# Performance work log

Measured on AMD Instinct MI355X. Metric: run time of the kernel, lower is better.

The kernel has to match this reference:

```python
import jax, jax.numpy as jnp
import numpy as np

DIM = 512
NUM_HEADS = 8


def setup_inputs() -> dict:
    key = jax.random.key(0)
    ks = jax.random.split(key, 10)
    B, N, C = 2, 4096, DIM
    s = 0.02
    return {
        "x": jax.random.normal(ks[0], (B, N, C), dtype=jnp.float32),
        "Wq": jax.random.normal(ks[1], (C, C), dtype=jnp.float32) * s,
        "Wk": jax.random.normal(ks[2], (C, C), dtype=jnp.float32) * s,
        "Wv": jax.random.normal(ks[3], (C, C), dtype=jnp.float32) * s,
        "Wattn": jax.random.normal(ks[4], (C, C), dtype=jnp.float32) * s,
        "Wconv": jax.random.normal(ks[5], (C, C), dtype=jnp.float32) * s,
        "dw_kernel": jax.random.normal(ks[6], (C, 1, 3), dtype=jnp.float32) * s,  # depthwise (O, I/groups, K)
        "dw_bias": jax.random.normal(ks[7], (C,), dtype=jnp.float32) * s,
        "Wcout": jax.random.normal(ks[8], (C, C), dtype=jnp.float32) * s,
        "H": 8,
        "W": 512,
    }


def reference(x, Wq, Wk, Wv, Wattn, Wconv, dw_kernel, dw_bias, Wcout, H, W):
    B, N, C = x.shape
    nh = NUM_HEADS
    hd = C // nh
    scale = hd ** (-0.5)

    # QKV projections (torch Linear: x @ W.T), split heads -> [B, nh, N, hd]
    q = (x @ Wq.T).reshape(B, N, nh, hd).transpose(0, 2, 1, 3)
    k = (x @ Wk.T).reshape(B, N, nh, hd).transpose(0, 2, 1, 3)
    v = (x @ Wv.T).reshape(B, N, nh, hd).transpose(0, 2, 1, 3)

    # Materialized N x N attention (faithful to source)
    scores = jnp.einsum("bhqd,bhkd->bhqk", q, k) * scale
    weights = jax.nn.softmax(scores, axis=-1)
    attn = jnp.einsum("bhqk,bhkd->bhqd", weights, v)
    attn = attn.transpose(0, 2, 1, 3).reshape(B, N, C)
    attn_out = attn @ Wattn.T

    # Parallel depthwise-conv branch
    ci = (x @ Wconv.T).transpose(0, 2, 1)  # [B, C, N]
    co = jax.lax.conv_general_dilated(
        ci, dw_kernel,
        window_strides=(1,), padding=((1, 1),),
        feature_group_count=C,
        dimension_numbers=("NCH", "OIH", "NCH"),
    ) + dw_bias[None, :, None]
    conv_out = co.transpose(0, 2, 1) @ Wcout.T  # [B, N, C]

    out = attn_out + conv_out
    # NOTE: source shadows arg H with num_heads before the view
    return out.reshape(B, nh, W, C)
```

## Files before the change

### kernel.cpp

```cpp
#include <hip/hip_runtime.h>

typedef __attribute__((ext_vector_type(8))) short bf16x8;
typedef __attribute__((ext_vector_type(4))) float f32x4;

constexpr int kB = 2, kN = 4096, kC = 512, kNH = 8, kHD = 64;
constexpr int kBN = kB * kN;
constexpr int kWElems = 262144;
constexpr int kWAll = 6 * kWElems;
constexpr int kWExtra = 3584;
constexpr float kQScale = 0.1803368801f;

__device__ __forceinline__ short f2bf(float f) {
  union { float f; unsigned u; } v; v.f = f;
  unsigned r = v.u + 0x7fffu + ((v.u >> 16) & 1u);
  return (short)(r >> 16);
}
__device__ __forceinline__ float bf2f(short s) {
  union { unsigned u; float f; } v; v.u = ((unsigned)(unsigned short)s) << 16;
  return v.f;
}
__device__ __forceinline__ float exp2_(float x) {
#if __has_builtin(__builtin_amdgcn_exp2f)
  return __builtin_amdgcn_exp2f(x);
#else
  return exp2f(x);
#endif
}
__device__ __forceinline__ unsigned pk2bf(float a, float b) {
  union { float f; unsigned u; } ua, ub; ua.f = a; ub.f = b;
#if __has_builtin(__builtin_amdgcn_perm)
  return __builtin_amdgcn_perm(ub.u + 0x8000u, ua.u + 0x8000u, 0x07060302u);
#else
  return ((ua.u + 0x8000u) >> 16) | (((ub.u + 0x8000u) >> 16) << 16);
#endif
}

__device__ __forceinline__ bf16x8 ld8(const short* p) { return *(const bf16x8*)p; }
__device__ __forceinline__ bf16x8 ld8(const float* p) {
  float4 a = *(const float4*)p;
  float4 b = *(const float4*)(p + 4);
  bf16x8 r;
  r[0] = f2bf(a.x); r[1] = f2bf(a.y); r[2] = f2bf(a.z); r[3] = f2bf(a.w);
  r[4] = f2bf(b.x); r[5] = f2bf(b.y); r[6] = f2bf(b.z); r[7] = f2bf(b.w);
  return r;
}

__device__ __forceinline__ void gload_lds16(const void* g, void* l) {
  __builtin_amdgcn_global_load_lds(
      (const __attribute__((address_space(1))) void*)g,
      (__attribute__((address_space(3))) void*)l, 16, 0, 0);
}

__global__ void detect_dtype(const unsigned* __restrict__ x, int* __restrict__ flag) {
  const int lane = threadIdx.x & 63;
  unsigned w = x[lane];
  int e = (int)((w >> 7) & 0xffu);
  bool bf = (e >= 100 && e <= 140);
  unsigned long long m = __ballot(bf);
  if (lane == 0) *flag = (__popcll(m) >= 32) ? 1 : 0;
}

constexpr int kW8 = kWAll / 8;
constexpr int kX8 = kBN * kC / 8;
__global__ __launch_bounds__(256) void convert_all(
    const void* Wq, const void* Wk, const void* Wv, const void* Wc,
    const void* Wa, const void* Wco, const void* dwk, const void* dwb,
    const void* x, const int* __restrict__ flag, short* __restrict__ dst,
    short* __restrict__ xb) {
  const int gtid = blockIdx.x * 256 + threadIdx.x;
  const bool bf = (*flag != 0);
  if (gtid < kW8) {
    const int e = gtid * 8;
    const int t = e >> 18, off = e & (kWElems - 1);
    const void* src = (t == 0) ? Wq : (t == 1) ? Wk : (t == 2) ? Wv
                    : (t == 3) ? Wc : (t == 4) ? Wa : Wco;
    bf16x8 v = bf ? ld8((const short*)src + off) : ld8((const float*)src + off);
    *(bf16x8*)(dst + e) = v;
  } else if (gtid < kW8 + kWExtra) {
    const int eoff = gtid - kW8;
    if (eoff < 1536) {
      dst[kWAll + eoff] = bf ? ((const short*)dwk)[eoff]
                             : f2bf(((const float*)dwk)[eoff]);
    } else if (eoff < 2048) {
      const int i = eoff - 1536;
      dst[kWAll + 1536 + i] = bf ? ((const short*)dwb)[i]
                                 : f2bf(((const float*)dwb)[i]);
    } else {
      const int t2 = eoff - 2048;
      const int tap = t2 >> 9, c = t2 & 511;
      dst[kWAll + 2048 + t2] = bf ? ((const short*)dwk)[c * 3 + tap]
                                  : f2bf(((const float*)dwk)[c * 3 + tap]);
    }
  } else if (gtid < kW8 + kWExtra + kX8) {
    const int e = (gtid - kW8 - kWExtra) * 8;
    bf16x8 v = bf ? ld8((const short*)x + e) : ld8((const float*)x + e);
    *(bf16x8*)(xb + e) = v;
  }
}

__global__ __launch_bounds__(256, 3) void proj_gemm(
    const short* __restrict__ xb, const short* __restrict__ wb,
    short* __restrict__ q, short* __restrict__ k, short* __restrict__ vT,
    short* __restrict__ ci) {
  __shared__ __align__(16) short Sh[16384];
  short* As = Sh;
  short* Bs = Sh + 8192;
  const int t = threadIdx.x;
  const int wave = t >> 6, lane = t & 63;
  const int row = lane & 15, quad = lane >> 4;
  const int bn = blockIdx.x & 15;
  const int bm = blockIdx.x >> 4;
  const int m0 = bm * 128, n0 = bn * 128;
  const int wm = wave & 1, wn = wave >> 1;
  const int lrow = lane >> 3, lch = lane & 7;

  f32x4 acc[4][4];
#pragma unroll
  for (int mi = 0; mi < 4; ++mi)
#pragma unroll
    for (int ni = 0; ni < 4; ++ni)
#pragma unroll
      for (int r = 0; r < 4; ++r) acc[mi][ni][r] = 0.0f;

  for (int k0 = 0; k0 < kC; k0 += 64) {
#pragma unroll
    for (int p = 0; p < 4; ++p) {
      const int m = wave * 32 + p * 8 + lrow;
      const int kch = lch ^ (m & 7);
      gload_lds16(xb + (size_t)(m0 + m) * kC + k0 + kch * 8,
                  &As[(wave * 32 + p * 8) * 64]);
      gload_lds16(wb + (size_t)(n0 + m) * kC + k0 + kch * 8,
                  &Bs[(wave * 32 + p * 8) * 64]);
    }
    __syncthreads();

#pragma unroll
    for (int kk2 = 0; kk2 < 2; ++kk2) {
      bf16x8 af[4], bfr[4];
#pragma unroll
      for (int mi = 0; mi < 4; ++mi) {
        const int m = wm * 64 + mi * 16 + row;
        const int ch = (kk2 * 4 + quad) ^ (m & 7);
        af[mi] = *(const bf16x8*)(&As[m * 64 + ch * 8]);
      }
#pragma unroll
      for (int ni = 0; ni < 4; ++ni) {
        const int n = wn * 64 + ni * 16 + row;
        const int ch = (kk2 * 4 + quad) ^ (n & 7);
        bfr[ni] = *(const bf16x8*)(&Bs[n * 64 + ch * 8]);
      }
#pragma unroll
      for (int mi = 0; mi < 4; ++mi)
#pragma unroll
        for (int ni = 0; ni < 4; ++ni)
          acc[mi][ni] = __builtin_amdgcn_mfma_f32_16x16x32_bf16(
              af[mi], bfr[ni], acc[mi][ni], 0, 0, 0);
    }
    __syncthreads();
  }

  const int mat = n0 >> 9;
  const float scale = (mat == 0) ? kQScale : 1.0f;
  if (mat != 2) {
#pragma unroll
    for (int mi = 0; mi < 4; ++mi)
#pragma unroll
      for (int ni = 0; ni < 4; ++ni)
#pragma unroll
        for (int r = 0; r < 4; ++r) {
          const int m = wm * 64 + mi * 16 + quad * 4 + r;
          const int n = wn * 64 + ni * 16 + row;
          Sh[m * 128 + (((n >> 3) ^ (m & 15)) * 8) + (n & 7)] =
              f2bf(acc[mi][ni][r] * scale);
        }
  } else {
#pragma unroll
    for (int mi = 0; mi < 4; ++mi)
#pragma unroll
      for (int ni = 0; ni < 4; ++ni)
#pragma unroll
        for (int r = 0; r < 4; ++r) {
          const int m = wm * 64 + mi * 16 + quad * 4 + r;
          const int n = wn * 64 + ni * 16 + row;
          Sh[n * 128 + (((m >> 3) ^ (n & 15)) * 8) + (m & 7)] =
              f2bf(acc[mi][ni][r]);
        }
  }
  __syncthreads();
  const int b_ = m0 >> 12;
  const int rsub = lane >> 4, chk = lane & 15;
#pragma unroll
  for (int i = 0; i < 8; ++i) {
    const int rr = i * 16 + wave * 4 + rsub;
    bf16x8 v = *(const bf16x8*)(&Sh[rr * 128 + ((chk ^ (rr & 15)) * 8)]);
    if (mat == 2) {
      const int cg = (n0 + rr) & 511;
      const int h = cg >> 6, d = cg & 63;
      const int nb = (m0 & (kN - 1)) + chk * 8;
      *(bf16x8*)(vT + ((size_t)((b_ * kNH + h) * kHD + d)) * kN + nb) = v;
    } else {
      const int n_ = (m0 & (kN - 1)) + rr;
      const int cg = (n0 + chk * 8) & 511;
      if (mat == 3) {
        *(bf16x8*)(ci + ((size_t)(b_ * kN + n_)) * kC + cg) = v;
      } else {
        const int h = cg >> 6, d = cg & 63;
        short* dst = (mat == 0) ? q : k;
        *(bf16x8*)(dst + ((size_t)((b_ * kNH + h) * kN + n_)) * kHD + d) = v;
      }
    }
  }
}

__global__ __launch_bounds__(256) void dwconv(
    const short* __restrict__ ci, const short* __restrict__ wb,
    short* __restrict__ cb) {
  const int e0 = (blockIdx.x * 256 + threadIdx.x) * 8;
  const int c0 = e0 & (kC - 1);
  const int bn = e0 >> 9;
  const int n_ = bn & (kN - 1);
  bf16x8 xc = ld8(ci + e0);
  bf16x8 xm, xp;
  if (n_ > 0) xm = ld8(ci + e0 - kC);
  else
#pragma unroll
    for (int i = 0; i < 8; ++i) xm[i] = 0;
  if (n_ < kN - 1) xp = ld8(ci + e0 + kC);
  else
#pragma unroll
    for (int i = 0; i < 8; ++i) xp[i] = 0;
  bf16x8 w0 = ld8(wb + kWAll + 2048 + c0);
  bf16x8 w1 = ld8(wb + kWAll + 2048 + 512 + c0);
  bf16x8 w2 = ld8(wb + kWAll + 2048 + 1024 + c0);
  bf16x8 bi = ld8(wb + kWAll + 1536 + c0);
  bf16x8 o;
#pragma unroll
  for (int i = 0; i < 8; ++i) {
    float a = bf2f(bi[i]) + bf2f(xm[i]) * bf2f(w0[i]) +
              bf2f(xc[i]) * bf2f(w1[i]) + bf2f(xp[i]) * bf2f(w2[i]);
    o[i] = f2bf(a);
  }
  *(bf16x8*)(cb + e0) = o;
}

__global__ __launch_bounds__(512, 2) void attn_flash(
    const short* __restrict__ q, const short* __restrict__ k,
    const short* __restrict__ vT, short* __restrict__ attn) {
  __shared__ __align__(16) short SMEM[34816];
  short* Kb = SMEM;
  short* Vb = SMEM + 16384;
  const int t = threadIdx.x;
  const int wave = t >> 6;
  const int lane = t & 63;
  const int row = lane & 15;
  const int quad = lane >> 4;
  const int qg = wave & 3;
  const int ks = wave >> 2;

  const int slot = blockIdx.x & 7;
  const int inner = blockIdx.x >> 3;
  const int bh = slot * 2 + (inner & 1);
  const int q0 = (inner >> 1) * 256 + qg * 64;

  const short* qbase = q + (size_t)(bh * kN + q0) * kHD;
  const short* kbase = k + (size_t)bh * kN * kHD;
  const short* vbase = vT + (size_t)bh * kHD * kN;

  bf16x8 qb[4][2];
#pragma unroll
  for (int g = 0; g < 4; ++g) {
    qb[g][0] = *(const bf16x8*)(qbase + (g * 16 + row) * kHD + quad * 8);
    qb[g][1] = *(const bf16x8*)(qbase + (g * 16 + row) * kHD + 32 + quad * 8);
  }

  const f32x4 z4 = {0.0f, 0.0f, 0.0f, 0.0f};

  f32x4 o[4][4];
#pragma unroll
  for (int g = 0; g < 4; ++g)
#pragma unroll
    for (int j = 0; j < 4; ++j)
#pragma unroll
      for (int r = 0; r < 4; ++r) o[g][j][r] = 0.0f;
  float l_[4] = {0.0f, 0.0f, 0.0f, 0.0f};

  const int ksrow = lane >> 3;
  const int kschunk = (lane & 7) ^ ksrow;
  auto stage_k = [&](int buf, int kt) {
#pragma unroll
    for (int s2 = 0; s2 < 2; ++s2)
      gload_lds16(
          kbase + (size_t)(s2 * 2048 + kt * 64 + wave * 8 + ksrow) * 64 +
              kschunk * 8,
          &Kb[(buf * 2 + s2) * 4096 + wave * 512]);
  };

  const int sv = t >> 8;
  const int ii = t & 255;
  const int i0 = ii, i1 = ii + 256;
  const int sr0 = i0 >> 3, sc0 = i0 & 7;
  const int sr1 = i1 >> 3, sc1 = i1 & 7;
  const int vb0 = (sc0 >> 2) * 32 + (sc0 & 1) * 16 + (sc0 & 2) * 2;
  const int vb1 = (sc1 >> 2) * 32 + (sc1 & 1) * 16 + (sc1 & 2) * 2;

  auto stage_v = [&](int buf, bf16x8 v0, bf16x8 v1) {
    short* base = &Vb[(buf * 2 + sv) * 4608];
    *(short4*)(&base[sr0 * 72 + vb0]) = make_short4(v0[0], v0[1], v0[2], v0[3]);
    *(short4*)(&base[sr0 * 72 + vb0 + 8]) = make_short4(v0[4], v0[5], v0[6], v0[7]);
    *(short4*)(&base[sr1 * 72 + vb1]) = make_short4(v1[0], v1[1], v1[2], v1[3]);
    *(short4*)(&base[sr1 * 72 + vb1 + 8]) = make_short4(v1[4], v1[5], v1[6], v1[7]);
  };

  const int c0s = ((quad) ^ (row & 7)) * 8;
  const int c1s = ((quad + 4) ^ (row & 7)) * 8;

  auto tile_step = [&](const short* kt_base, const short* vt_base) {
    f32x4 s[4][4];
    __builtin_amdgcn_s_setprio(1);
#pragma unroll
    for (int jk = 0; jk < 4; ++jk) {
      const short* kr = kt_base + (jk * 16 + row) * 64;
      bf16x8 a0 = *(const bf16x8*)(kr + c0s);
      bf16x8 a1 = *(const bf16x8*)(kr + c1s);
#pragma unroll
      for (int g = 0; g < 4; ++g) {
        s[g][jk] = __builtin_amdgcn_mfma_f32_16x16x32_bf16(a0, qb[g][0], z4, 0, 0, 0);
        s[g][jk] = __builtin_amdgcn_mfma_f32_16x16x32_bf16(a1, qb[g][1], s[g][jk], 0, 0, 0);
      }
    }
    __builtin_amdgcn_s_setprio(0);

    bf16x8 pb[4][2];
#pragma unroll
    for (int g = 0; g < 4; ++g) {
      float tj[4];
#pragma unroll
      for (int jk = 0; jk < 4; ++jk) {
#pragma unroll
        for (int r = 0; r < 4; ++r) s[g][jk][r] = exp2_(s[g][jk][r]);
        tj[jk] = (s[g][jk][0] + s[g][jk][1]) + (s[g][jk][2] + s[g][jk][3]);
      }
      l_[g] += (tj[0] + tj[1]) + (tj[2] + tj[3]);
#pragma unroll
      for (int c = 0; c < 2; ++c) {
        union { unsigned u[4]; bf16x8 v; } pu;
        pu.u[0] = pk2bf(s[g][2 * c][0], s[g][2 * c][1]);
        pu.u[1] = pk2bf(s[g][2 * c][2], s[g][2 * c][3]);
        pu.u[2] = pk2bf(s[g][2 * c + 1][0], s[g][2 * c + 1][1]);
        pu.u[3] = pk2bf(s[g][2 * c + 1][2], s[g][2 * c + 1][3]);
        pb[g][c] = pu.v;
      }
    }

    __builtin_amdgcn_s_setprio(1);
#pragma unroll
    for (int jd = 0; jd < 4; ++jd) {
      const short* vb = vt_base + (jd * 16 + row) * 72 + quad * 8;
#pragma unroll
      for (int c = 0; c < 2; ++c) {
        bf16x8 av = *(const bf16x8*)(vb + c * 32);
#pragma unroll
        for (int g = 0; g < 4; ++g)
          o[g][jd] = __builtin_amdgcn_mfma_f32_16x16x32_bf16(
              av, pb[g][c], o[g][jd], 0, 0, 0);
      }
    }
    __builtin_amdgcn_s_setprio(0);
  };

  {
    stage_k(0, 0);
    bf16x8 a = *(const bf16x8*)(vbase + (size_t)sr0 * kN + sv * 2048 + sc0 * 8);
    bf16x8 b = *(const bf16x8*)(vbase + (size_t)sr1 * kN + sv * 2048 + sc1 * 8);
    stage_v(0, a, b);
  }
  __syncthreads();

  for (int kt = 0; kt < 32; ++kt) {
    const int cur = kt & 1;
    const bool more = (kt < 31);
    bf16x8 vn0, vn1;
    if (more) {
      stage_k(1 - cur, kt + 1);
      const int off = sv * 2048 + (kt + 1) * 64;
      vn0 = *(const bf16x8*)(vbase + (size_t)sr0 * kN + off + sc0 * 8);
      vn1 = *(const bf16x8*)(vbase + (size_t)sr1 * kN + off + sc1 * 8);
    }

    tile_step(&Kb[(cur * 2 + ks) * 4096], &Vb[(cur * 2 + ks) * 4608]);

    if (more) stage_v(1 - cur, vn0, vn1);
    __syncthreads();
  }

  float* Of = (float*)SMEM;
  float* Lf = (float*)SMEM + 16384;
  if (ks == 1) {
#pragma unroll
    for (int g = 0; g < 4; ++g) {
#pragma unroll
      for (int jd = 0; jd < 4; ++jd)
#pragma unroll
        for (int r = 0; r < 4; ++r)
          Of[(g * 16 + jd * 4 + r) * 256 + qg * 64 + lane] = o[g][jd][r];
      Lf[g * 256 + qg * 64 + lane] = l_[g];
    }
  }
  __syncthreads();
  if (ks == 0) {
#pragma unroll
    for (int g = 0; g < 4; ++g) {
#pragma unroll
      for (int jd = 0; jd < 4; ++jd)
#pragma unroll
        for (int r = 0; r < 4; ++r)
          o[g][jd][r] += Of[(g * 16 + jd * 4 + r) * 256 + qg * 64 + lane];
      l_[g] += Lf[g * 256 + qg * 64 + lane];
    }
    const int b_ = bh >> 3, h = bh & 7;
#pragma unroll
    for (int g = 0; g < 4; ++g) {
      float lt = l_[g];
      lt += __shfl_xor(lt, 16);
      lt += __shfl_xor(lt, 32);
      const float linv = 1.0f / lt;
      const int n_ = q0 + g * 16 + row;
      short* ob = attn + (size_t)(b_ * kN + n_) * kC + h * kHD + quad * 4;
#pragma unroll
      for (int jd = 0; jd < 4; ++jd) {
        short4 st = make_short4(f2bf(o[g][jd][0] * linv), f2bf(o[g][jd][1] * linv),
                                f2bf(o[g][jd][2] * linv), f2bf(o[g][jd][3] * linv));
        *(short4*)(ob + jd * 16) = st;
      }
    }
  }
}

template <typename TO>
__device__ __forceinline__ void out_body(
    const short* __restrict__ attn, const short* __restrict__ cb,
    const short* __restrict__ wb, TO* __restrict__ out) {
  __shared__ __align__(16) short Sh[16384];
  short* As = Sh;
  short* Bs = Sh + 8192;
  const int t = threadIdx.x;
  const int wave = t >> 6, lane = t & 63;
  const int row = lane & 15, quad = lane >> 4;
  const int bn = blockIdx.x & 7;
  const int bm = blockIdx.x >> 3;
  const int m0 = bm * 128, n0 = bn * 64;
  const int wm = wave & 1, wn = wave >> 1;
  const int lrow = lane >> 3, lch = lane & 7;

  f32x4 acc[4][2];
#pragma unroll
  for (int mi = 0; mi < 4; ++mi)
#pragma unroll
    for (int ni = 0; ni < 2; ++ni)
#pragma unroll
      for (int r = 0; r < 4; ++r) acc[mi][ni][r] = 0.0f;

  const short* Wa = wb + 4 * kWElems;
  const short* Wo = wb + 5 * kWElems;

  for (int k0 = 0; k0 < 1024; k0 += 64) {
    const short* Asrc = (k0 < 512) ? attn : cb;
    const short* Bsrc = (k0 < 512) ? Wa : Wo;
    const int ka = k0 & 511;
#pragma unroll
    for (int p = 0; p < 4; ++p) {
      const int m = wave * 32 + p * 8 + lrow;
      const int kch = lch ^ (m & 7);
      gload_lds16(Asrc + (size_t)(m0 + m) * kC + ka + kch * 8,
                  &As[(wave * 32 + p * 8) * 64]);
    }
#pragma unroll
    for (int p = 0; p < 2; ++p) {
      const int n = wave * 16 + p * 8 + lrow;
      const int kch = lch ^ (n & 7);
      gload_lds16(Bsrc + (size_t)(n0 + n) * kC + ka + kch * 8,
                  &Bs[(wave * 16 + p * 8) * 64]);
    }
    __syncthreads();

#pragma unroll
    for (int kk2 = 0; kk2 < 2; ++kk2) {
      bf16x8 af[4], bfr[2];
#pragma unroll
      for (int mi = 0; mi < 4; ++mi) {
        const int m = wm * 64 + mi * 16 + row;
        const int ch = (kk2 * 4 + quad) ^ (m & 7);
        af[mi] = *(const bf16x8*)(&As[m * 64 + ch * 8]);
      }
#pragma unroll
      for (int ni = 0; ni < 2; ++ni) {
        const int n = wn * 32 + ni * 16 + row;
        const int ch = (kk2 * 4 + quad) ^ (n & 7);
        bfr[ni] = *(const bf16x8*)(&Bs[n * 64 + ch * 8]);
      }
#pragma unroll
      for (int mi = 0; mi < 4; ++mi)
#pragma unroll
        for (int ni = 0; ni < 2; ++ni)
          acc[mi][ni] = __builtin_amdgcn_mfma_f32_16x16x32_bf16(
              af[mi], bfr[ni], acc[mi][ni], 0, 0, 0);
    }
    __syncthreads();
  }

  if constexpr (sizeof(TO) == 4) {
    float* Shf = (float*)Sh;
#pragma unroll
    for (int mi = 0; mi < 4; ++mi)
#pragma unroll
      for (int ni = 0; ni < 2; ++ni)
#pragma unroll
        for (int r = 0; r < 4; ++r) {
          const int m = wm * 64 + mi * 16 + quad * 4 + r;
          const int n = wn * 32 + ni * 16 + row;
          Shf[m * 64 + (((n >> 2) ^ (m & 15)) * 4) + (n & 3)] = acc[mi][ni][r];
        }
    __syncthreads();
    const int rsub = lane >> 4, chk = lane & 15;
#pragma unroll
    for (int i = 0; i < 8; ++i) {
      const int rr = i * 16 + wave * 4 + rsub;
      float4 v = *(const float4*)(&Shf[rr * 64 + ((chk ^ (rr & 15)) * 4)]);
      *(float4*)((float*)out + (size_t)(m0 + rr) * kC + n0 + chk * 4) = v;
    }
  } else {
#pragma unroll
    for (int mi = 0; mi < 4; ++mi)
#pragma unroll
      for (int ni = 0; ni < 2; ++ni)
#pragma unroll
        for (int r = 0; r < 4; ++r) {
          const int m = wm * 64 + mi * 16 + quad * 4 + r;
          const int n = wn * 32 + ni * 16 + row;
          Sh[m * 64 + (((n >> 3) ^ (m & 7)) * 8) + (n & 7)] =
              f2bf(acc[mi][ni][r]);
        }
    __syncthreads();
    const int rsub = lane >> 3, chk = lane & 7;
#pragma unroll
    for (int i = 0; i < 4; ++i) {
      const int rr = i * 32 + wave * 8 + rsub;
      bf16x8 v = *(const bf16x8*)(&Sh[rr * 64 + ((chk ^ (rr & 7)) * 8)]);
      *(bf16x8*)((short*)out + (size_t)(m0 + rr) * kC + n0 + chk * 8) = v;
    }
  }
}

__global__ __launch_bounds__(256, 4) void out_gemm(
    const short* __restrict__ attn, const short* __restrict__ cb,
    const short* __restrict__ wb, const int* __restrict__ flag, void* out) {
  if (*flag)
    out_body<short>(attn, cb, wb, (short*)out);
  else
    out_body<float>(attn, cb, wb, (float*)out);
}

extern "C" void kernel_launch(void* const* d_in, const int* in_sizes, int n_in,
                              void* d_out, int out_size, void* d_ws, size_t ws_size,
                              hipStream_t stream) {
  const void* x   = d_in[0];
  const void* Wq  = d_in[1];
  const void* Wk  = d_in[2];
  const void* Wv  = d_in[3];
  const void* Wa  = d_in[4];
  const void* Wc  = d_in[5];
  const void* dwk = d_in[6];
  const void* dwb = d_in[7];
  const void* Wco = d_in[8];

  short* ws = (short*)d_ws;
  const size_t E = (size_t)kBN * kC;
  int*   flag = (int*)ws;
  short* wb   = ws + 256;
  short* q    = wb + kWAll + kWExtra;
  short* k    = q + E;
  short* vT   = k + E;
  short* ci   = vT + E;
  short* cb   = ci + E;
  short* attn = ci;
  short* xb   = cb;

  detect_dtype<<<1, 64, 0, stream>>>((const unsigned*)x, flag);
  const int cvt_threads = kW8 + kWExtra + kX8;
  convert_all<<<(cvt_threads + 255) / 256, 256, 0, stream>>>(
      Wq, Wk, Wv, Wc, Wa, Wco, dwk, dwb, x, flag, wb, xb);
  proj_gemm<<<1024, 256, 0, stream>>>(xb, wb, q, k, vT, ci);
  dwconv<<<(kBN * kC) / (256 * 8), 256, 0, stream>>>(ci, wb, cb);
  attn_flash<<<256, 512, 0, stream>>>(q, k, vT, attn);
  out_gemm<<<512, 256, 0, stream>>>(attn, cb, wb, flag, d_out);
}
```

Measured before the change: 214.9 us.

## Process two KV tiles per barrier in flash attention and swizzle GEMM block order

The attention kernel now stages two 64-key K/V tiles per double-buffer slot. It runs two tile steps between barriers, halving the number of __syncthreads and giving each prefetch a longer window to overlap with compute. LDS use doubles to about 136 KB per block, which may affect whether two 512-thread blocks fit per CU. Separately, the projection and output GEMMs remap block indices with an XCD-aware swizzle, so that neighbouring tiles land on the same chiplet and share L2.

```diff
diff --git a/kernel.cpp b/kernel.cpp
--- a/kernel.cpp
+++ b/kernel.cpp
@@ -108,8 +108,9 @@
   const int t = threadIdx.x;
   const int wave = t >> 6, lane = t & 63;
   const int row = lane & 15, quad = lane >> 4;
-  const int bn = blockIdx.x & 15;
-  const int bm = blockIdx.x >> 4;
+  const int swz = (blockIdx.x & 7) * 128 + (blockIdx.x >> 3);
+  const int bn = swz & 15;
+  const int bm = swz >> 4;
   const int m0 = bm * 128, n0 = bn * 128;
   const int wm = wave & 1, wn = wave >> 1;
   const int lrow = lane >> 3, lch = lane & 7;
@@ -246,9 +247,9 @@
 __global__ __launch_bounds__(512, 2) void attn_flash(
     const short* __restrict__ q, const short* __restrict__ k,
     const short* __restrict__ vT, short* __restrict__ attn) {
-  __shared__ __align__(16) short SMEM[34816];
+  __shared__ __align__(16) short SMEM[69632];
   short* Kb = SMEM;
-  short* Vb = SMEM + 16384;
+  short* Vb = SMEM + 32768;
   const int t = threadIdx.x;
   const int wave = t >> 6;
   const int lane = t & 63;
@@ -286,13 +287,15 @@
 
   const int ksrow = lane >> 3;
   const int kschunk = (lane & 7) ^ ksrow;
-  auto stage_k = [&](int buf, int kt) {
-#pragma unroll
-    for (int s2 = 0; s2 < 2; ++s2)
-      gload_lds16(
-          kbase + (size_t)(s2 * 2048 + kt * 64 + wave * 8 + ksrow) * 64 +
-              kschunk * 8,
-          &Kb[(buf * 2 + s2) * 4096 + wave * 512]);
+  auto stage_k = [&](int buf, int ktbase) {
+#pragma unroll
+    for (int tl = 0; tl < 2; ++tl)
+#pragma unroll
+      for (int s2 = 0; s2 < 2; ++s2)
+        gload_lds16(
+            kbase + (size_t)(s2 * 2048 + (ktbase + tl) * 64 + wave * 8 + ksrow) * 64 +
+                kschunk * 8,
+            &Kb[((buf * 2 + tl) * 2 + s2) * 4096 + wave * 512]);
   };
 
   const int sv = t >> 8;
@@ -303,8 +306,8 @@
   const int vb0 = (sc0 >> 2) * 32 + (sc0 & 1) * 16 + (sc0 & 2) * 2;
   const int vb1 = (sc1 >> 2) * 32 + (sc1 & 1) * 16 + (sc1 & 2) * 2;
 
-  auto stage_v = [&](int buf, bf16x8 v0, bf16x8 v1) {
-    short* base = &Vb[(buf * 2 + sv) * 4608];
+  auto stage_v = [&](int buf, int tl, bf16x8 v0, bf16x8 v1) {
+    short* base = &Vb[((buf * 2 + tl) * 2 + sv) * 4608];
     *(short4*)(&base[sr0 * 72 + vb0]) = make_short4(v0[0], v0[1], v0[2], v0[3]);
     *(short4*)(&base[sr0 * 72 + vb0 + 8]) = make_short4(v0[4], v0[5], v0[6], v0[7]);
     *(short4*)(&base[sr1 * 72 + vb1]) = make_short4(v1[0], v1[1], v1[2], v1[3]);
@@ -370,26 +373,36 @@
 
   {
     stage_k(0, 0);
-    bf16x8 a = *(const bf16x8*)(vbase + (size_t)sr0 * kN + sv * 2048 + sc0 * 8);
-    bf16x8 b = *(const bf16x8*)(vbase + (size_t)sr1 * kN + sv * 2048 + sc1 * 8);
-    stage_v(0, a, b);
+#pragma unroll
+    for (int tl = 0; tl < 2; ++tl) {
+      bf16x8 a = *(const bf16x8*)(vbase + (size_t)sr0 * kN + sv * 2048 + tl * 64 + sc0 * 8);
+      bf16x8 b = *(const bf16x8*)(vbase + (size_t)sr1 * kN + sv * 2048 + tl * 64 + sc1 * 8);
+      stage_v(0, tl, a, b);
+    }
   }
   __syncthreads();
 
-  for (int kt = 0; kt < 32; ++kt) {
-    const int cur = kt & 1;
-    const bool more = (kt < 31);
-    bf16x8 vn0, vn1;
+  for (int p = 0; p < 16; ++p) {
+    const int cur = p & 1;
+    const bool more = (p < 15);
+    bf16x8 vn00, vn01, vn10, vn11;
     if (more) {
-      stage_k(1 - cur, kt + 1);
-      const int off = sv * 2048 + (kt + 1) * 64;
-      vn0 = *(const bf16x8*)(vbase + (size_t)sr0 * kN + off + sc0 * 8);
-      vn1 = *(const bf16x8*)(vbase + (size_t)sr1 * kN + off + sc1 * 8);
-    }
-
-    tile_step(&Kb[(cur * 2 + ks) * 4096], &Vb[(cur * 2 + ks) * 4608]);
-
-    if (more) stage_v(1 - cur, vn0, vn1);
+      stage_k(1 - cur, 2 * p + 2);
+      const int off = sv * 2048 + (2 * p + 2) * 64;
+      vn00 = *(const bf16x8*)(vbase + (size_t)sr0 * kN + off + sc0 * 8);
+      vn01 = *(const bf16x8*)(vbase + (size_t)sr1 * kN + off + sc1 * 8);
+      vn10 = *(const bf16x8*)(vbase + (size_t)sr0 * kN + off + 64 + sc0 * 8);
+      vn11 = *(const bf16x8*)(vbase + (size_t)sr1 * kN + off + 64 + sc1 * 8);
+    }
+
+    tile_step(&Kb[((cur * 2 + 0) * 2 + ks) * 4096], &Vb[((cur * 2 + 0) * 2 + ks) * 4608]);
+
+    if (more) {
+      stage_v(1 - cur, 0, vn00, vn01);
+      stage_v(1 - cur, 1, vn10, vn11);
+    }
+
+    tile_step(&Kb[((cur * 2 + 1) * 2 + ks) * 4096], &Vb[((cur * 2 + 1) * 2 + ks) * 4608]);
     __syncthreads();
   }
 
@@ -446,8 +459,9 @@
   const int t = threadIdx.x;
   const int wave = t >> 6, lane = t & 63;
   const int row = lane & 15, quad = lane >> 4;
-  const int bn = blockIdx.x & 7;
-  const int bm = blockIdx.x >> 3;
+  const int swz = (blockIdx.x & 7) * 64 + (blockIdx.x >> 3);
+  const int bn = swz & 7;
+  const int bm = swz >> 3;
   const int m0 = bm * 128, n0 = bn * 64;
   const int wm = wave & 1, wn = wave >> 1;
   const int lrow = lane >> 3, lch = lane & 7;
```

After: 215.6 us. About the same (+0.3%).
